# Optimization experiments

Hardware: AMD Instinct MI355X
Metric: run time of the kernel (lower is better)

The kernel has to match this reference:

```python
import jax, jax.numpy as jnp
import numpy as np

HEADS = 32
KV_HEADS = 8
HEAD_DIM = 128
ROPE_THETA = 10000.0


def _rope_tables(position_ids, head_dim, dtype):
    # position_ids: [S] int
    inv_freq = 1.0 / (ROPE_THETA ** (jnp.arange(0, head_dim, 2, dtype=jnp.float32) / head_dim))
    freqs = position_ids.astype(jnp.float32)[:, None] * inv_freq[None, :]   # [S, hd/2]
    emb = jnp.concatenate([freqs, freqs], axis=-1)                          # [S, hd]
    return jnp.cos(emb).astype(dtype), jnp.sin(emb).astype(dtype)


def _rotate_half(x):
    h = x.shape[-1] // 2
    return jnp.concatenate([-x[..., h:], x[..., :h]], axis=-1)


def setup_inputs() -> dict:
    key = jax.random.key(0)
    ks = jax.random.split(key, 5)
    B, S, D = 2, 2048, 4096
    kv_dim = KV_HEADS * HEAD_DIM
    s = 0.02
    return {
        "hidden_states": jax.random.normal(ks[0], (B, S, D), jnp.float32),
        "position_ids": jnp.arange(S, dtype=jnp.int64 if jax.config.jax_enable_x64 else jnp.int32),
        "wq": jax.random.normal(ks[1], (D, D), jnp.float32) * s,
        "wk": jax.random.normal(ks[2], (kv_dim, D), jnp.float32) * s,
        "wv": jax.random.normal(ks[3], (kv_dim, D), jnp.float32) * s,
        "wo": jax.random.normal(ks[4], (D, D), jnp.float32) * s,
    }


def reference(hidden_states, position_ids, wq, wk, wv, wo):
    B, S, D = hidden_states.shape
    groups = HEADS // KV_HEADS

    # Q/K/V projections (nn.Linear: x @ W.T), split into heads -> [B, H, S, hd]
    q = (hidden_states @ wq.T).reshape(B, S, HEADS, HEAD_DIM).transpose(0, 2, 1, 3)
    k = (hidden_states @ wk.T).reshape(B, S, KV_HEADS, HEAD_DIM).transpose(0, 2, 1, 3)
    v = (hidden_states @ wv.T).reshape(B, S, KV_HEADS, HEAD_DIM).transpose(0, 2, 1, 3)

    # RoPE
    cos, sin = _rope_tables(position_ids, HEAD_DIM, q.dtype)  # [S, hd]
    q = q * cos + _rotate_half(q) * sin
    k = k * cos + _rotate_half(k) * sin

    # GQA: expand KV heads to match Q heads
    k = jnp.repeat(k, groups, axis=1)  # [B, H, S, hd]
    v = jnp.repeat(v, groups, axis=1)

    # causal SDPA
    scale = 1.0 / jnp.sqrt(jnp.asarray(HEAD_DIM, q.dtype))
    scores = jnp.einsum("bhqd,bhkd->bhqk", q, k) * scale
    causal = jnp.tril(jnp.ones((S, S), dtype=bool))
    scores = jnp.where(causal, scores, jnp.finfo(scores.dtype).min)
    probs = jax.nn.softmax(scores, axis=-1)
    attn = jnp.einsum("bhqk,bhkd->bhqd", probs, v)  # [B, H, S, hd]

    # merge heads + output projection
    attn = attn.transpose(0, 2, 1, 3).reshape(B, S, D)
    return attn @ wo.T
```

## Files before the change

kernel.cpp:

```cpp
#include <hip/hip_runtime.h>
#include <hip/hip_bf16.h>
#include <math.h>

typedef __attribute__((ext_vector_type(8))) short short8;
typedef __attribute__((ext_vector_type(4))) float f32x4;
typedef __attribute__((ext_vector_type(16))) float f32x16;
typedef __attribute__((ext_vector_type(4))) unsigned int u32x4;
typedef __attribute__((ext_vector_type(2))) int i32x2;

#define BATCH   2
#define SLEN    2048
#define DMODEL  4096
#define NHEADS  32
#define KVHEADS 8
#define HD      128
#define KVDIM   (KVHEADS*HD)
#define MROWS   (BATCH*SLEN)
#define NQKV    (DMODEL + 2*KVDIM)

#define GLDS16(gp, lp) __builtin_amdgcn_global_load_lds( \
    (const __attribute__((address_space(1))) void*)(gp), \
    (__attribute__((address_space(3))) void*)(lp), 16, 0, 0)

static __device__ __forceinline__ unsigned short bf16bits(float x) {
    __hip_bfloat16 h = __float2bfloat16(x);
    return *(unsigned short*)&h;
}
static __device__ __forceinline__ float bf2f(unsigned short u) {
    __hip_bfloat16 h = *(__hip_bfloat16*)&u;
    return __bfloat162float(h);
}
static __device__ __forceinline__ unsigned cvtpk(float a, float b) {
    unsigned r;
    asm("v_cvt_pk_bf16_f32 %0, %1, %2" : "=v"(r) : "v"(a), "v"(b));
    return r;
}

__global__ __launch_bounds__(256) void cast_k(const float* __restrict__ in,
                                              unsigned short* __restrict__ out, long n) {
    long i = ((long)blockIdx.x * 256 + threadIdx.x) * 4;
    if (i >= n) return;
    float4 v = *(const float4*)(in + i);
    union { unsigned short h[4]; uint2 u; } c;
    c.h[0] = bf16bits(v.x); c.h[1] = bf16bits(v.y);
    c.h[2] = bf16bits(v.z); c.h[3] = bf16bits(v.w);
    *(uint2*)(out + i) = c.u;
}

__global__ void rope_table_k(const int* __restrict__ pos,
                             float* __restrict__ cosT, float* __restrict__ sinT) {
    int s = blockIdx.x;
    int d = threadIdx.x;
    float p = (float)pos[s];
    float inv = powf(10000.0f, -(float)(2 * d) / 128.0f);
    float ang = p * inv;
    cosT[s * 64 + d] = cosf(ang);
    sinT[s * 64 + d] = sinf(ang);
}

__global__ void rope_bf_k(unsigned short* __restrict__ x,
                          const float* __restrict__ cosT, const float* __restrict__ sinT,
                          int nh, int ld, float mul) {
    int idx = blockIdx.x * 256 + threadIdx.x;
    int d = idx & 63;
    int rest = idx >> 6;
    int h = rest % nh;
    int row = rest / nh;
    int s = row & (SLEN - 1);
    float c  = cosT[s * 64 + d] * mul;
    float sn = sinT[s * 64 + d] * mul;
    unsigned short* base = x + (size_t)row * ld + h * HD;
    float x1 = bf2f(base[d]), x2 = bf2f(base[d + 64]);
    base[d]      = bf16bits(x1 * c - x2 * sn);
    base[d + 64] = bf16bits(x2 * c + x1 * sn);
}

__global__ __launch_bounds__(256) void vtrans_k(const unsigned short* __restrict__ V, int ldv,
                                                unsigned short* __restrict__ Vt) {
    __shared__ unsigned short L[64][144];
    const int t = threadIdx.x;
    const int s0 = blockIdx.x * 64;
    const int bk = blockIdx.y;
    const int b = bk >> 3, kvh = bk & 7;
    #pragma unroll
    for (int j = 0; j < 4; ++j) {
        int idx = t + j * 256;
        int row = idx >> 4;
        int c8  = (idx & 15) * 8;
        *(short8*)&L[row][c8] =
            *(const short8*)(V + ((size_t)b * SLEN + s0 + row) * ldv + kvh * HD + c8);
    }
    __syncthreads();
    {
        int d  = t >> 1;
        int sh = (t & 1) * 32;
        unsigned short tmp[32];
        #pragma unroll
        for (int j = 0; j < 32; ++j) tmp[j] = L[sh + j][d];
        unsigned short* dst = Vt + ((size_t)bk * HD + d) * SLEN + s0 + sh;
        #pragma unroll
        for (int j = 0; j < 4; ++j)
            *(short8*)(dst + j * 8) = *(const short8*)(tmp + j * 8);
    }
}

template<typename CT>
__global__ __launch_bounds__(512, 1) void gemm256(
    const unsigned short* __restrict__ A, int lda,
    const unsigned short* __restrict__ W, int ldw,
    CT* __restrict__ C, int ldc,
    int M, int N, int K)
{
    __shared__ unsigned short Asl[2][2][128 * 64];
    __shared__ unsigned short Bsl[2][2][128 * 64];

    const int t = threadIdx.x;
    const int w = t >> 6, lane = t & 63;

    const int gx = gridDim.x;
    const int nwg = gx * gridDim.y;
    const int orig = blockIdx.y * gx + blockIdx.x;
    const int swzid = (orig & 7) * (nwg >> 3) + (orig >> 3);
    const int m0 = (swzid / gx) * 256, n0 = (swzid % gx) * 256;

    const int wm = (w >> 2) * 128;
    const int wn = (w & 3) * 64;
    const int fr = lane & 15, hi = lane >> 4;

    f32x4 acc[8][4];
    #pragma unroll
    for (int i = 0; i < 8; ++i)
        #pragma unroll
        for (int j = 0; j < 4; ++j)
            acc[i][j] = (f32x4){0.f, 0.f, 0.f, 0.f};

    const int sr = t >> 3;
    const int sl = t & 7;
    const int wv512 = w * 512;

    {
        #pragma unroll
        for (int hh = 0; hh < 4; ++hh) {
            #pragma unroll
            for (int j = 0; j < 2; ++j) {
                const int row = j * 64 + sr;
                const int scol = (sl ^ (row & 7)) << 3;
                if (hh < 2)
                    GLDS16(W + (size_t)(n0 + hh * 128 + row) * ldw + scol,
                           &Bsl[0][hh][j * 4096 + wv512]);
                else
                    GLDS16(A + (size_t)(m0 + (hh - 2) * 128 + row) * lda + scol,
                           &Asl[0][hh - 2][j * 4096 + wv512]);
            }
        }
        asm volatile("s_waitcnt vmcnt(2)" ::: "memory");
        __builtin_amdgcn_s_barrier();
        __builtin_amdgcn_sched_barrier(0);
    }

    const int NT = K >> 6;
    int buf = 0;
    for (int kt = 0; kt < NT; ++kt) {
        const unsigned short* Ah = Asl[buf][w >> 2];
        const unsigned short* Bh = Bsl[buf][(w & 3) >> 1];
        const bool pf = (kt + 1 < NT);
        const int k0n = (kt + 1) << 6;
        short8 bfr[4][2];

        #pragma unroll
        for (int q = 0; q < 4; ++q) {
            if (q == 0) {
                #pragma unroll
                for (int j = 0; j < 4; ++j) {
                    const int lr = (wn & 127) + j * 16 + fr;
                    const int sz = lr & 7;
                    bfr[j][0] = *(const short8*)&Bh[lr * 64 + (((0 + hi) ^ sz) << 3)];
                    bfr[j][1] = *(const short8*)&Bh[lr * 64 + (((4 + hi) ^ sz) << 3)];
                }
            }
            short8 af[2][2];
            #pragma unroll
            for (int ii = 0; ii < 2; ++ii) {
                const int lr = q * 32 + ii * 16 + fr;
                const int sz = lr & 7;
                af[ii][0] = *(const short8*)&Ah[lr * 64 + (((0 + hi) ^ sz) << 3)];
                af[ii][1] = *(const short8*)&Ah[lr * 64 + (((4 + hi) ^ sz) << 3)];
            }

            if (pf) {
                #pragma unroll
                for (int j = 0; j < 2; ++j) {
                    const int row = j * 64 + sr;
                    const int scol = k0n + ((sl ^ (row & 7)) << 3);
                    if (q < 2)
                        GLDS16(W + (size_t)(n0 + q * 128 + row) * ldw + scol,
                               &Bsl[buf ^ 1][q][j * 4096 + wv512]);
                    else
                        GLDS16(A + (size_t)(m0 + (q - 2) * 128 + row) * lda + scol,
                               &Asl[buf ^ 1][q - 2][j * 4096 + wv512]);
                }
            }

            __builtin_amdgcn_sched_barrier(0);
            __builtin_amdgcn_s_barrier();
            __builtin_amdgcn_sched_barrier(0);

            __builtin_amdgcn_s_setprio(1);
            #pragma unroll
            for (int ii = 0; ii < 2; ++ii)
                #pragma unroll
                for (int j = 0; j < 4; ++j) {
                    acc[q * 2 + ii][j] = __builtin_amdgcn_mfma_f32_16x16x32_bf16(
                        af[ii][0], bfr[j][0], acc[q * 2 + ii][j], 0, 0, 0);
                    acc[q * 2 + ii][j] = __builtin_amdgcn_mfma_f32_16x16x32_bf16(
                        af[ii][1], bfr[j][1], acc[q * 2 + ii][j], 0, 0, 0);
                }
            __builtin_amdgcn_s_setprio(0);

            if (q == 1) {
                if (pf) asm volatile("s_waitcnt vmcnt(4)" ::: "memory");
                else    asm volatile("s_waitcnt vmcnt(0)" ::: "memory");
            } else if (q == 3 && pf) {
                asm volatile("s_waitcnt vmcnt(2)" ::: "memory");
            }
            __builtin_amdgcn_sched_barrier(0);
            __builtin_amdgcn_s_barrier();
            __builtin_amdgcn_sched_barrier(0);
        }
        buf ^= 1;
    }

    const int crow = (lane >> 4) * 4, ccol = lane & 15;
    #pragma unroll
    for (int i = 0; i < 8; ++i)
        #pragma unroll
        for (int j = 0; j < 4; ++j) {
            CT* cp = C + (size_t)(m0 + wm + i * 16 + crow) * ldc + (n0 + wn + j * 16 + ccol);
            #pragma unroll
            for (int r = 0; r < 4; ++r) {
                if constexpr (sizeof(CT) == 2)
                    cp[(size_t)r * ldc] = bf16bits(acc[i][j][r]);
                else
                    cp[(size_t)r * ldc] = acc[i][j][r];
            }
        }
}

__global__ __launch_bounds__(256, 2) void flash_mfma32(
    const unsigned short* __restrict__ Qb, int ldq,
    const unsigned short* __restrict__ Kb, int ldk,
    const unsigned short* __restrict__ Vt,
    unsigned short* __restrict__ Ob)
{
    __shared__ unsigned short Ks[2][64 * 128];
    __shared__ unsigned short Vs[2][128 * 64];

    const int t = threadIdx.x;
    const int wid = t >> 6, lane = t & 63;
    const int qt = (int)gridDim.x - 1 - (int)blockIdx.x;
    const int bh = blockIdx.y;
    const int b = bh >> 5, h = bh & 31, kvh = h >> 2;
    const int lq = lane & 31;
    const int hl = lane >> 5;
    const int qw0 = qt * 128 + wid * 32;
    const int qg = qw0 + lq;
    const size_t qrowg = (size_t)b * SLEN + qg;

    const unsigned short* Kg0 = Kb + (size_t)b * SLEN * ldk + kvh * HD;
    const unsigned short* Vg0 = Vt + (size_t)(b * KVHEADS + kvh) * HD * SLEN;

    auto STAGE = [&](int buf, int kt) {
        const unsigned short* Kg = Kg0 + (size_t)kt * 64 * ldk;
        #pragma unroll
        for (int i = 0; i < 4; ++i) {
            int row = i * 16 + (t >> 4);
            int colel = ((((t & 15) << 4) ^ ((row & 15) << 4)) >> 1);
            GLDS16(Kg + (size_t)row * ldk + colel, &Ks[buf][i * 2048 + wid * 512]);
        }
        const unsigned short* Vg = Vg0 + kt * 64;
        #pragma unroll
        for (int i = 0; i < 4; ++i) {
            int row = i * 32 + (t >> 3);
            int colel = ((((t & 7) << 4) ^ ((row & 7) << 4)) >> 1);
            GLDS16(Vg + (size_t)row * SLEN + colel, &Vs[buf][i * 2048 + wid * 512]);
        }
    };

    STAGE(0, 0);
    short8 qf[8];
    {
        const unsigned short* qp = Qb + qrowg * ldq + h * HD + hl * 8;
        #pragma unroll
        for (int dt = 0; dt < 8; ++dt)
            qf[dt] = *(const short8*)(qp + dt * 16);
    }

    f32x16 accO[4];
    #pragma unroll
    for (int db = 0; db < 4; ++db)
        #pragma unroll
        for (int r = 0; r < 16; ++r) accO[db][r] = 0.f;
    float m_i = -INFINITY, l_i = 0.f;

    const int ntmax = 2 * qt + 2;
    int p = 0;
    for (int kt = 0; kt < ntmax; ++kt) {
        if (kt + 1 < ntmax) {
            STAGE(p ^ 1, kt + 1);
            asm volatile("s_waitcnt vmcnt(8)" ::: "memory");
        } else {
            asm volatile("s_waitcnt vmcnt(0)" ::: "memory");
        }
        __builtin_amdgcn_s_barrier();
        __builtin_amdgcn_sched_barrier(0);

        const unsigned short* Kp = Ks[p];
        const unsigned short* Vp = Vs[p];

        f32x16 sc[2];
        #pragma unroll
        for (int blk = 0; blk < 2; ++blk) {
            #pragma unroll
            for (int r = 0; r < 16; ++r) sc[blk][r] = 0.f;
            __builtin_amdgcn_s_setprio(1);
            #pragma unroll
            for (int dt = 0; dt < 8; ++dt) {
                int krow = blk * 32 + lq;
                int kb = krow * 256 + ((dt * 32 + hl * 16) ^ ((krow & 15) << 4));
                short8 kf = *(const short8*)(Kp + (kb >> 1));
                sc[blk] = __builtin_amdgcn_mfma_f32_32x32x16_bf16(kf, qf[dt], sc[blk], 0, 0, 0);
            }
            __builtin_amdgcn_s_setprio(0);
        }

        if (kt * 64 + 63 > qw0) {
            #pragma unroll
            for (int blk = 0; blk < 2; ++blk)
                #pragma unroll
                for (int r = 0; r < 16; ++r) {
                    int kv = kt * 64 + blk * 32 + (r & 3) + 8 * (r >> 2) + 4 * hl;
                    if (kv > qg) sc[blk][r] = -INFINITY;
                }
        }

        float pmax = sc[0][0];
        #pragma unroll
        for (int r = 1; r < 16; ++r) pmax = fmaxf(pmax, sc[0][r]);
        #pragma unroll
        for (int r = 0; r < 16; ++r) pmax = fmaxf(pmax, sc[1][r]);
        {
            i32x2 mr = __builtin_amdgcn_permlane32_swap(__float_as_int(pmax), __float_as_int(pmax), false, false);
            pmax = fmaxf(__int_as_float(mr.x), __int_as_float(mr.y));
        }

        if (!__all(pmax <= m_i + 8.0f)) {
            float mn = fmaxf(m_i, pmax);
            float al = exp2f(m_i - mn);
            m_i = mn;
            l_i *= al;
            #pragma unroll
            for (int db = 0; db < 4; ++db)
                #pragma unroll
                for (int r = 0; r < 16; ++r) accO[db][r] *= al;
        }

        float rs = 0.f;
        #pragma unroll
        for (int blk = 0; blk < 2; ++blk)
            #pragma unroll
            for (int r = 0; r < 16; ++r) {
                float pv = exp2f(sc[blk][r] - m_i);
                sc[blk][r] = pv;
                rs += pv;
            }
        {
            i32x2 sr = __builtin_amdgcn_permlane32_swap(__float_as_int(rs), __float_as_int(rs), false, false);
            rs = __int_as_float(sr.x) + __int_as_float(sr.y);
        }
        l_i += rs;

        short8 pf[4];
        #pragma unroll
        for (int blk = 0; blk < 2; ++blk) {
            unsigned c01 = cvtpk(sc[blk][0],  sc[blk][1]);
            unsigned c23 = cvtpk(sc[blk][2],  sc[blk][3]);
            unsigned c45 = cvtpk(sc[blk][4],  sc[blk][5]);
            unsigned c67 = cvtpk(sc[blk][6],  sc[blk][7]);
            i32x2 sA = __builtin_amdgcn_permlane32_swap((int)c01, (int)c45, false, false);
            i32x2 sB = __builtin_amdgcn_permlane32_swap((int)c23, (int)c67, false, false);
            u32x4 f0 = {(unsigned)sA.x, (unsigned)sB.x, (unsigned)sA.y, (unsigned)sB.y};
            pf[blk * 2] = *(short8*)&f0;
            unsigned c89 = cvtpk(sc[blk][8],  sc[blk][9]);
            unsigned cab = cvtpk(sc[blk][10], sc[blk][11]);
            unsigned ccd = cvtpk(sc[blk][12], sc[blk][13]);
            unsigned cef = cvtpk(sc[blk][14], sc[blk][15]);
            i32x2 sC = __builtin_amdgcn_permlane32_swap((int)c89, (int)ccd, false, false);
            i32x2 sD = __builtin_amdgcn_permlane32_swap((int)cab, (int)cef, false, false);
            u32x4 f1 = {(unsigned)sC.x, (unsigned)sD.x, (unsigned)sC.y, (unsigned)sD.y};
            pf[blk * 2 + 1] = *(short8*)&f1;
        }

        #pragma unroll
        for (int db = 0; db < 4; ++db) {
            __builtin_amdgcn_s_setprio(1);
            #pragma unroll
            for (int ks = 0; ks < 4; ++ks) {
                int vrow = db * 32 + lq;
                int vb = vrow * 128 + ((ks * 32 + hl * 16) ^ ((vrow & 7) << 4));
                short8 vf = *(const short8*)(Vp + (vb >> 1));
                accO[db] = __builtin_amdgcn_mfma_f32_32x32x16_bf16(vf, pf[ks], accO[db], 0, 0, 0);
            }
            __builtin_amdgcn_s_setprio(0);
        }

        __builtin_amdgcn_sched_barrier(0);
        __builtin_amdgcn_s_barrier();
        p ^= 1;
    }

    float inv = 1.0f / l_i;
    unsigned short* orow = Ob + qrowg * DMODEL + h * HD;
    #pragma unroll
    for (int db = 0; db < 4; ++db)
        #pragma unroll
        for (int rq = 0; rq < 4; ++rq) {
            unsigned w0 = cvtpk(accO[db][rq * 4 + 0] * inv, accO[db][rq * 4 + 1] * inv);
            unsigned w1 = cvtpk(accO[db][rq * 4 + 2] * inv, accO[db][rq * 4 + 3] * inv);
            uint2 pkd; pkd.x = w0; pkd.y = w1;
            *(uint2*)(orow + db * 32 + rq * 8 + hl * 4) = pkd;
        }
}

extern "C" void kernel_launch(void* const* d_in, const int* in_sizes, int n_in,
                              void* d_out, int out_size, void* d_ws, size_t ws_size,
                              hipStream_t stream) {
    const float* hs  = (const float*)d_in[0];
    const int*   pos = (const int*)d_in[1];
    const float* wq  = (const float*)d_in[2];
    const float* wk  = (const float*)d_in[3];
    const float* wv  = (const float*)d_in[4];
    const float* wo  = (const float*)d_in[5];
    float* out = (float*)d_out;

    char* ws = (char*)d_ws;
    unsigned short* hs_bf   = (unsigned short*)(ws);
    unsigned short* wqkv_bf = (unsigned short*)(ws + ((size_t)32  << 20));
    unsigned short* wo_bf   = (unsigned short*)(ws + ((size_t)80  << 20));
    unsigned short* qkv_bf  = (unsigned short*)(ws + ((size_t)112 << 20));
    unsigned short* Vtb     = (unsigned short*)(ws + ((size_t)160 << 20));
    unsigned short* Obf     = (unsigned short*)(ws + ((size_t)168 << 20));
    float*          cosT    = (float*)(ws + ((size_t)200 << 20));
    float*          sinT    = (float*)(ws + ((size_t)200 << 20) + (size_t)SLEN * 64 * 4);

    const long nHS = (long)MROWS * DMODEL;
    const long nWQ = (long)DMODEL * DMODEL;
    const long nWK = (long)KVDIM * DMODEL;

    rope_table_k<<<SLEN, 64, 0, stream>>>(pos, cosT, sinT);

    cast_k<<<nHS / 4 / 256, 256, 0, stream>>>(hs, hs_bf, nHS);
    cast_k<<<nWQ / 4 / 256, 256, 0, stream>>>(wq, wqkv_bf, nWQ);
    cast_k<<<nWK / 4 / 256, 256, 0, stream>>>(wk, wqkv_bf + (size_t)DMODEL * DMODEL, nWK);
    cast_k<<<nWK / 4 / 256, 256, 0, stream>>>(wv, wqkv_bf + (size_t)(DMODEL + KVDIM) * DMODEL, nWK);
    cast_k<<<nWQ / 4 / 256, 256, 0, stream>>>(wo, wo_bf, nWQ);

    gemm256<unsigned short><<<dim3(NQKV/256, MROWS/256), 512, 0, stream>>>(
        hs_bf, DMODEL, wqkv_bf, DMODEL, qkv_bf, NQKV, MROWS, NQKV, DMODEL);

    const float qmul = 0.088388347648318447f * 1.4426950408889634f;
    rope_bf_k<<<(MROWS * NHEADS  * 64) / 256, 256, 0, stream>>>(qkv_bf,          cosT, sinT, NHEADS,  NQKV, qmul);
    rope_bf_k<<<(MROWS * KVHEADS * 64) / 256, 256, 0, stream>>>(qkv_bf + DMODEL, cosT, sinT, KVHEADS, NQKV, 1.0f);
    vtrans_k<<<dim3(SLEN/64, BATCH*KVHEADS), 256, 0, stream>>>(qkv_bf + DMODEL + KVDIM, NQKV, Vtb);

    flash_mfma32<<<dim3(SLEN/128, BATCH*NHEADS), 256, 0, stream>>>(
        qkv_bf, NQKV, qkv_bf + DMODEL, NQKV, Vtb, Obf);

    gemm256<float><<<dim3(DMODEL/256, MROWS/256), 512, 0, stream>>>(
        Obf, DMODEL, wo_bf, DMODEL, out, DMODEL, MROWS, DMODEL, DMODEL);
}
```

Measured before the change: 635.6 us.

## Remap GEMM tiles to 2D per-XCD regions and restructure prefetch waits

Result: slower. 651.1 us (+2.4%).

```diff
diff --git a/kernel.cpp b/kernel.cpp
--- a/kernel.cpp
+++ b/kernel.cpp
@@ -119,9 +119,15 @@
 
     const int gx = gridDim.x;
     const int nwg = gx * gridDim.y;
+    const int chunk = nwg >> 3;
     const int orig = blockIdx.y * gx + blockIdx.x;
-    const int swzid = (orig & 7) * (nwg >> 3) + (orig >> 3);
-    const int m0 = (swzid / gx) * 256, n0 = (swzid % gx) * 256;
+    const int xcd = orig & 7, idx = orig >> 3;
+    const int rn = chunk >> 3;
+    const int nrx = gx / rn;
+    const int rx = xcd % nrx, ry = xcd / nrx;
+    const int iy = idx / rn, ix = idx % rn;
+    const int m0 = (ry * 8 + iy) * 256;
+    const int n0 = (rx * rn + ix) * 256;
 
     const int wm = (w >> 2) * 128;
     const int wn = (w & 3) * 64;
@@ -153,7 +159,7 @@
                            &Asl[0][hh - 2][j * 4096 + wv512]);
             }
         }
-        asm volatile("s_waitcnt vmcnt(2)" ::: "memory");
+        asm volatile("s_waitcnt vmcnt(0)" ::: "memory");
         __builtin_amdgcn_s_barrier();
         __builtin_amdgcn_sched_barrier(0);
     }
@@ -188,16 +194,24 @@
             }
 
             if (pf) {
-                #pragma unroll
-                for (int j = 0; j < 2; ++j) {
-                    const int row = j * 64 + sr;
-                    const int scol = k0n + ((sl ^ (row & 7)) << 3);
-                    if (q < 2)
+                if (q < 2) {
+                    #pragma unroll
+                    for (int j = 0; j < 2; ++j) {
+                        const int row = j * 64 + sr;
+                        const int scol = k0n + ((sl ^ (row & 7)) << 3);
                         GLDS16(W + (size_t)(n0 + q * 128 + row) * ldw + scol,
                                &Bsl[buf ^ 1][q][j * 4096 + wv512]);
-                    else
-                        GLDS16(A + (size_t)(m0 + (q - 2) * 128 + row) * lda + scol,
-                               &Asl[buf ^ 1][q - 2][j * 4096 + wv512]);
+                    }
+                } else if (q == 2) {
+                    #pragma unroll
+                    for (int half = 0; half < 2; ++half)
+                        #pragma unroll
+                        for (int j = 0; j < 2; ++j) {
+                            const int row = j * 64 + sr;
+                            const int scol = k0n + ((sl ^ (row & 7)) << 3);
+                            GLDS16(A + (size_t)(m0 + half * 128 + row) * lda + scol,
+                                   &Asl[buf ^ 1][half][j * 4096 + wv512]);
+                        }
                 }
             }
 
@@ -217,12 +231,9 @@
                 }
             __builtin_amdgcn_s_setprio(0);
 
-            if (q == 1) {
-                if (pf) asm volatile("s_waitcnt vmcnt(4)" ::: "memory");
-                else    asm volatile("s_waitcnt vmcnt(0)" ::: "memory");
-            } else if (q == 3 && pf) {
-                asm volatile("s_waitcnt vmcnt(2)" ::: "memory");
-            }
+            if (q == 3 && pf)
+                asm volatile("s_waitcnt vmcnt(0)" ::: "memory");
+
             __builtin_amdgcn_sched_barrier(0);
             __builtin_amdgcn_s_barrier();
             __builtin_amdgcn_sched_barrier(0);
```
